# Kernel optimization log

Hardware: AMD Instinct MI355X
Metric: run time of the kernel (lower is better)

## Reference

```python
import jax, jax.numpy as jnp
import numpy as np

N_NODES = 10000
N_EDGES = 160000
DIM_IN = 32
DIM_OUT = 64
DIM_EDGE_HIDDEN = 128
BOND_FDIM = 13


def setup_inputs() -> dict:
    key = jax.random.key(0)
    ks = jax.random.split(key, 10)
    s = 0.1
    x = jax.random.normal(ks[0], (N_NODES, DIM_IN), dtype=jnp.float32)
    edge_index = jax.random.randint(ks[1], (2, N_EDGES), 0, N_NODES, dtype=jnp.int64)
    edge_attr = jax.random.uniform(ks[2], (N_EDGES, BOND_FDIM), dtype=jnp.float32)
    # edge-MLP params: BOND_FDIM -> hidden -> in*out
    W1 = jax.random.normal(ks[3], (BOND_FDIM, DIM_EDGE_HIDDEN), dtype=jnp.float32) * s
    b1 = jnp.zeros((DIM_EDGE_HIDDEN,), dtype=jnp.float32)
    W2 = jax.random.normal(ks[4], (DIM_EDGE_HIDDEN, DIM_IN * DIM_OUT), dtype=jnp.float32) * s
    b2 = jnp.zeros((DIM_IN * DIM_OUT,), dtype=jnp.float32)
    # NNConv root weight + bias
    root = jax.random.normal(ks[5], (DIM_IN, DIM_OUT), dtype=jnp.float32) * s
    bias = jnp.zeros((DIM_OUT,), dtype=jnp.float32)
    return {"x": x, "edge_index": edge_index, "edge_attr": edge_attr,
            "W1": W1, "b1": b1, "W2": W2, "b2": b2, "root": root, "bias": bias}


def reference(x, edge_index, edge_attr, W1, b1, W2, b2, root, bias):
    src, dst = edge_index[0], edge_index[1]  # PyG: row=source j, col=target i
    # edge MLP -> per-edge weight matrix [E, in, out]
    h = jax.nn.relu(edge_attr @ W1 + b1)
    w = (h @ W2 + b2).reshape(-1, DIM_IN, DIM_OUT)
    # gather source features, per-edge matmul -> messages [E, out]
    msg = jnp.einsum('ei,eio->eo', x[src], w)
    # scatter-add to target nodes
    agg = jax.ops.segment_sum(msg, dst, num_segments=N_NODES)
    out = agg + x @ root + bias
    return jax.nn.relu(out)
```

## Files before the change

kernel.cpp:

```cpp
#include <hip/hip_runtime.h>

#define N_NODES 10000
#define N_EDGES 160000
#define DIM_IN 32
#define DIM_OUT 64
#define DIM_HID 128
#define BOND 13
#define NB 16
#define NGROUPS (N_NODES / NB)
#define CAP 96

typedef _Float16 half2_t __attribute__((ext_vector_type(2)));
typedef _Float16 f16x8 __attribute__((ext_vector_type(8)));
typedef float f32x4 __attribute__((ext_vector_type(4)));
typedef unsigned int uint;

static __device__ __forceinline__ uint packh2(float a, float b) {
    half2_t h;
    h.x = (_Float16)a; h.y = (_Float16)b;
    return __builtin_bit_cast(uint, h);
}

static __device__ __forceinline__ int swz(int o, int kp) { return (o + kp) & 63; }

struct EScr {
    _Float16 ea16[16][32];
    _Float16 hbuf16[16][136];
};

__global__ void prep_kernel(const float* __restrict__ W2, uint4* __restrict__ W2p,
                            const float* __restrict__ W1, uint4* __restrict__ W1p,
                            const int* __restrict__ ei, int* __restrict__ cnt,
                            uint* __restrict__ es,
                            const float* __restrict__ x, const float* __restrict__ root,
                            const float* __restrict__ bias, float* __restrict__ out) {
    int idx = blockIdx.x * 256 + threadIdx.x;
    if (idx < 512 * 64) {
        int f = idx >> 6, lane = idx & 63;
        int k = f >> 2, of = f & 3;
        int q = lane >> 4, l15 = lane & 15;
        const float* base = W2 + k * 2048 + q * 512 + of * 16 + l15;
        uint u0 = packh2(base[0],   base[64]);
        uint u1 = packh2(base[128], base[192]);
        uint u2 = packh2(base[256], base[320]);
        uint u3 = packh2(base[384], base[448]);
        W2p[idx] = make_uint4(u0, u1, u2, u3);
    }
    if (idx < 512) {
        int nh = idx >> 6, lane = idx & 63;
        int quad = lane >> 4, l15 = lane & 15;
        int col = nh * 16 + l15;
        uint u[4];
#pragma unroll
        for (int jp = 0; jp < 4; ++jp) {
            int k0 = quad * 8 + 2 * jp, k1 = k0 + 1;
            float f0 = (k0 < BOND) ? W1[k0 * DIM_HID + col] : 0.f;
            float f1 = (k1 < BOND) ? W1[k1 * DIM_HID + col] : 0.f;
            u[jp] = packh2(f0, f1);
        }
        W1p[idx] = make_uint4(u[0], u[1], u[2], u[3]);
    }
    if (idx < N_NODES * DIM_OUT) {
        int n = idx >> 6, o = idx & 63;
        float r = bias[o];
        const float* xn = x + n * DIM_IN;
#pragma unroll 8
        for (int i = 0; i < DIM_IN; ++i) r += xn[i] * root[i * DIM_OUT + o];
        out[idx] = r;
    }
    if (idx < N_EDGES) {
        int src = ei[idx];
        int dst = ei[N_EDGES + idx];
        int slot = atomicAdd(&cnt[src], 1);
        if (slot < CAP)
            es[src * CAP + slot] = ((uint)dst << 18) | (uint)idx;
    }
}

__global__ __launch_bounds__(1024)
__attribute__((amdgpu_waves_per_eu(4, 4)))
void phase1_kernel(
    const float* __restrict__ x,
    const float* __restrict__ ea, const uint4* __restrict__ W1p,
    const float* __restrict__ b1, const uint4* __restrict__ W2p,
    const float* __restrict__ b2, const int* __restrict__ cnt,
    const uint* __restrict__ es, float* __restrict__ out)
{
    __shared__ uint  PhH[NB][DIM_HID / 4][DIM_OUT];
    __shared__ uint4 w1lds[8][64];

    const int t  = threadIdx.x;
    const int o  = t & 63;
    const int w  = t >> 6;
    const int n0 = blockIdx.x * NB;
    const int l15  = o & 15;
    const int quad = o >> 4;
    const int nd = w;
    const int n  = n0 + nd;

    if (t < 512) w1lds[t >> 6][t & 63] = W1p[t];

    const int start = n * CAP;
    int deg = cnt[n];
    uint pk = 0;
    if (o < 16) pk = es[start + o];

    f16x8 af;
    {
        uint ua[4];
        const float* xn8 = x + (long)(n0 + l15) * DIM_IN;
#pragma unroll
        for (int jj = 0; jj < 4; ++jj)
            ua[jj] = packh2(xn8[quad * 8 + 2 * jj], xn8[quad * 8 + 2 * jj + 1]);
        af = __builtin_bit_cast(f16x8, make_uint4(ua[0], ua[1], ua[2], ua[3]));
    }

    deg = deg < CAP ? deg : CAP;
    float eav[4];
    {
        const int tcnt0 = deg < 16 ? deg : 16;
#pragma unroll
        for (int r = 0; r < 4; ++r) {
            const int p = quad + 4 * r;
            const uint epk = __shfl(pk, p);
            eav[r] = 0.f;
            if (p < tcnt0 && l15 < BOND)
                eav[r] = ea[(long)(epk & 0x3FFFFu) * BOND + l15];
        }
    }

    f16x8 pregf[16];
    const int of = w & 3;
    const int ks = w >> 2;
#pragma unroll
    for (int h = 0; h < 2; ++h) {
        const int oo = of * 16 + l15;
        const int kbase = h * 64 + ks * 16;
#pragma unroll 2
        for (int m = 0; m < 8; ++m) {
            const int k0 = kbase + 2 * m;
            const uint4 bu0 = W2p[(k0 * 4 + of) * 64 + o];
            const uint4 bu1 = W2p[((k0 + 1) * 4 + of) * 64 + o];
            f32x4 D0 = {0.f, 0.f, 0.f, 0.f};
            f32x4 D1 = {0.f, 0.f, 0.f, 0.f};
            D0 = __builtin_amdgcn_mfma_f32_16x16x32_f16(
                     af, __builtin_bit_cast(f16x8, bu0), D0, 0, 0, 0);
            D1 = __builtin_amdgcn_mfma_f32_16x16x32_f16(
                     af, __builtin_bit_cast(f16x8, bu1), D1, 0, 0, 0);
            const int kpg = (kbase >> 1) + m;
            const int kpl = kpg & 31;
            const int sc = swz(oo, kpg);
#pragma unroll
            for (int r = 0; r < 4; ++r)
                PhH[quad * 4 + r][kpl][sc] = packh2(D0[r], D1[r]);
        }
        __syncthreads();
#pragma unroll
        for (int nt = 0; nt < 4; ++nt)
#pragma unroll
            for (int kh = 0; kh < 2; ++kh) {
                const int kk = 2 * h + kh;
                const int col = nt * 16 + l15;
                const int kpl = kh * 16 + quad * 4;
                const int kpg = h * 32 + kpl;
                uint4 u;
                u.x = PhH[nd][kpl + 0][swz(col, kpg + 0)];
                u.y = PhH[nd][kpl + 1][swz(col, kpg + 1)];
                u.z = PhH[nd][kpl + 2][swz(col, kpg + 2)];
                u.w = PhH[nd][kpl + 3][swz(col, kpg + 3)];
                pregf[nt * 4 + kk] = __builtin_bit_cast(f16x8, u);
            }
        __syncthreads();
    }

    float qv[4] = {0.f, 0.f, 0.f, 0.f};
    {
        const float* xn = x + (long)n * DIM_IN;
#pragma unroll 4
        for (int i = 0; i < DIM_IN; ++i) {
            float xv = xn[i];
#pragma unroll
            for (int nt = 0; nt < 4; ++nt)
                qv[nt] += xv * b2[i * DIM_OUT + nt * 16 + l15];
        }
    }

    float b1v[8];
#pragma unroll
    for (int nh = 0; nh < 8; ++nh) b1v[nh] = b1[nh * 16 + l15];

    EScr* S = (EScr*)((char*)&PhH[0][0][0] + nd * 8192);

    ((uint4*)S->ea16)[o] = make_uint4(0u, 0u, 0u, 0u);
    __builtin_amdgcn_wave_barrier();

    const int ntiles = (deg + 15) >> 4;
#pragma unroll 1
    for (int tb = 0; tb < ntiles; ++tb) {
        const int tilebase = tb * 16;
        const int tcnt = (deg - tilebase < 16) ? (deg - tilebase) : 16;
        __builtin_amdgcn_wave_barrier();
        if (l15 < BOND) {
#pragma unroll
            for (int r = 0; r < 4; ++r) {
                const int p = quad + 4 * r;
                if (p < tcnt) S->ea16[p][l15] = (_Float16)eav[r];
            }
        }
        __builtin_amdgcn_wave_barrier();
        const uint pkc = pk;

        uint pk2 = 0;
        float eav2[4] = {0.f, 0.f, 0.f, 0.f};
        const int tb2 = tilebase + 16;
        if (tb2 < deg) {
            const int tcnt2 = (deg - tb2 < 16) ? (deg - tb2) : 16;
            if (o < 16) pk2 = es[start + tb2 + o];
#pragma unroll
            for (int r = 0; r < 4; ++r) {
                const int p = quad + 4 * r;
                const uint epk = __shfl(pk2, p);
                if (p < tcnt2 && l15 < BOND)
                    eav2[r] = ea[(long)(epk & 0x3FFFFu) * BOND + l15];
            }
        }

        uint woff = 0;
        asm volatile("" : "+v"(woff));
        const int wo = (o + (int)woff) & 63;
        const f16x8 aef = *(const f16x8*)&S->ea16[l15][quad * 8];
#pragma unroll
        for (int nh = 0; nh < 8; ++nh) {
            const f16x8 wf = __builtin_bit_cast(f16x8, w1lds[nh][wo]);
            f32x4 hacc = {0.f, 0.f, 0.f, 0.f};
            hacc = __builtin_amdgcn_mfma_f32_16x16x32_f16(aef, wf, hacc, 0, 0, 0);
#pragma unroll
            for (int r = 0; r < 4; ++r) {
                float hv = hacc[r] + b1v[nh];
                S->hbuf16[quad * 4 + r][nh * 16 + l15] =
                    (_Float16)(hv > 0.f ? hv : 0.f);
            }
        }
        __builtin_amdgcn_wave_barrier();
        f16x8 hf[4];
#pragma unroll
        for (int kk = 0; kk < 4; ++kk)
            hf[kk] = *(const f16x8*)&S->hbuf16[l15][kk * 32 + quad * 8];
#pragma unroll
        for (int nt = 0; nt < 4; ++nt) {
            f32x4 acc = {0.f, 0.f, 0.f, 0.f};
#pragma unroll
            for (int kk = 0; kk < 4; ++kk)
                acc = __builtin_amdgcn_mfma_f32_16x16x32_f16(
                          hf[kk], pregf[nt * 4 + kk], acc, 0, 0, 0);
#pragma unroll
            for (int r = 0; r < 4; ++r) {
                const int p = quad * 4 + r;
                const uint dpk = __shfl(pkc, p);
                if (p < tcnt)
                    atomicAdd(&out[(long)(dpk >> 18) * DIM_OUT + nt * 16 + l15],
                              acc[r] + qv[nt]);
            }
        }
        pk = pk2;
#pragma unroll
        for (int r = 0; r < 4; ++r) eav[r] = eav2[r];
    }
}

__global__ __launch_bounds__(256) void relu_kernel(float* __restrict__ out) {
    int idx = blockIdx.x * 256 + threadIdx.x;
    if (idx < N_NODES * DIM_OUT) {
        float v = out[idx];
        out[idx] = v > 0.f ? v : 0.f;
    }
}


extern "C" void kernel_launch(void* const* d_in, const int* in_sizes, int n_in,
                              void* d_out, int out_size, void* d_ws, size_t ws_size,
                              hipStream_t stream) {
    const float* x    = (const float*)d_in[0];
    const int*   ei   = (const int*)d_in[1];
    const float* ea   = (const float*)d_in[2];
    const float* W1   = (const float*)d_in[3];
    const float* b1   = (const float*)d_in[4];
    const float* W2   = (const float*)d_in[5];
    const float* b2   = (const float*)d_in[6];
    const float* root = (const float*)d_in[7];
    const float* bias = (const float*)d_in[8];
    float* out = (float*)d_out;
    char* ws = (char*)d_ws;

    int*   cnt = (int*)(ws + 0);
    uint*  es  = (uint*)(ws + 40064);
    uint4* W2p = (uint4*)(ws + 3880064);
    uint4* W1p = (uint4*)(ws + 4404352);

    hipMemsetAsync(cnt, 0, 40064, stream);
    prep_kernel<<<2500, 256, 0, stream>>>(W2, W2p, W1, W1p, ei, cnt, es,
                                          x, root, bias, out);
    phase1_kernel<<<NGROUPS, 1024, 0, stream>>>(x, ea, W1p, b1, W2p, b2,
                                                cnt, es, out);
    relu_kernel<<<2500, 256, 0, stream>>>(out);
}
```

Baseline: 171.0 us.

## Fuse prep, edge conv and relu into one persistent kernel with grid barriers

Replaces the three kernel launches with a single persistent kernel of 256 blocks. Software grid barriers separate the prep phase (weight packing, edge bucketing) from a phase that pulls node groups from an atomic work counter, and then from a final phase that adds the root/bias term and applies relu. Messages now accumulate into a separate zeroed buffer instead of into the output, which needs a larger memset. This removes launch gaps and dynamically balances node groups, at the cost of spin-wait barriers, a larger memset, and relying on all 256 blocks being co-resident.

```diff
diff --git a/kernel.cpp b/kernel.cpp
--- a/kernel.cpp
+++ b/kernel.cpp
@@ -9,6 +9,7 @@
 #define NB 16
 #define NGROUPS (N_NODES / NB)
 #define CAP 96
+#define NBLK 256
 
 typedef _Float16 half2_t __attribute__((ext_vector_type(2)));
 typedef _Float16 f16x8 __attribute__((ext_vector_type(8)));
@@ -28,251 +29,265 @@
     _Float16 hbuf16[16][136];
 };
 
-__global__ void prep_kernel(const float* __restrict__ W2, uint4* __restrict__ W2p,
-                            const float* __restrict__ W1, uint4* __restrict__ W1p,
-                            const int* __restrict__ ei, int* __restrict__ cnt,
-                            uint* __restrict__ es,
-                            const float* __restrict__ x, const float* __restrict__ root,
-                            const float* __restrict__ bias, float* __restrict__ out) {
-    int idx = blockIdx.x * 256 + threadIdx.x;
-    if (idx < 512 * 64) {
-        int f = idx >> 6, lane = idx & 63;
-        int k = f >> 2, of = f & 3;
-        int q = lane >> 4, l15 = lane & 15;
-        const float* base = W2 + k * 2048 + q * 512 + of * 16 + l15;
-        uint u0 = packh2(base[0],   base[64]);
-        uint u1 = packh2(base[128], base[192]);
-        uint u2 = packh2(base[256], base[320]);
-        uint u3 = packh2(base[384], base[448]);
-        W2p[idx] = make_uint4(u0, u1, u2, u3);
+static __device__ __forceinline__ void gbar(int* ctr) {
+    __threadfence();
+    __syncthreads();
+    if (threadIdx.x == 0) {
+        atomicAdd(ctr, 1);
+        while (atomicAdd(ctr, 0) < NBLK) __builtin_amdgcn_s_sleep(16);
     }
-    if (idx < 512) {
-        int nh = idx >> 6, lane = idx & 63;
-        int quad = lane >> 4, l15 = lane & 15;
-        int col = nh * 16 + l15;
-        uint u[4];
-#pragma unroll
-        for (int jp = 0; jp < 4; ++jp) {
-            int k0 = quad * 8 + 2 * jp, k1 = k0 + 1;
-            float f0 = (k0 < BOND) ? W1[k0 * DIM_HID + col] : 0.f;
-            float f1 = (k1 < BOND) ? W1[k1 * DIM_HID + col] : 0.f;
-            u[jp] = packh2(f0, f1);
-        }
-        W1p[idx] = make_uint4(u[0], u[1], u[2], u[3]);
-    }
-    if (idx < N_NODES * DIM_OUT) {
-        int n = idx >> 6, o = idx & 63;
-        float r = bias[o];
-        const float* xn = x + n * DIM_IN;
-#pragma unroll 8
-        for (int i = 0; i < DIM_IN; ++i) r += xn[i] * root[i * DIM_OUT + o];
-        out[idx] = r;
-    }
-    if (idx < N_EDGES) {
-        int src = ei[idx];
-        int dst = ei[N_EDGES + idx];
-        int slot = atomicAdd(&cnt[src], 1);
-        if (slot < CAP)
-            es[src * CAP + slot] = ((uint)dst << 18) | (uint)idx;
-    }
+    __syncthreads();
+    __threadfence();
 }
 
 __global__ __launch_bounds__(1024)
 __attribute__((amdgpu_waves_per_eu(4, 4)))
-void phase1_kernel(
-    const float* __restrict__ x,
-    const float* __restrict__ ea, const uint4* __restrict__ W1p,
-    const float* __restrict__ b1, const uint4* __restrict__ W2p,
-    const float* __restrict__ b2, const int* __restrict__ cnt,
-    const uint* __restrict__ es, float* __restrict__ out)
+void fused_kernel(
+    const float* __restrict__ x,  const int* __restrict__ ei,
+    const float* __restrict__ ea, const float* __restrict__ W1,
+    const float* __restrict__ b1, const float* __restrict__ W2,
+    const float* __restrict__ b2, const float* __restrict__ root,
+    const float* __restrict__ bias,
+    int* __restrict__ ctrl, int* __restrict__ cnt,
+    float* __restrict__ accbuf, uint* __restrict__ es,
+    uint4* __restrict__ W2p, uint4* __restrict__ W1p,
+    float* __restrict__ out)
 {
     __shared__ uint  PhH[NB][DIM_HID / 4][DIM_OUT];
     __shared__ uint4 w1lds[8][64];
+    __shared__ int   gsh;
 
     const int t  = threadIdx.x;
     const int o  = t & 63;
     const int w  = t >> 6;
-    const int n0 = blockIdx.x * NB;
     const int l15  = o & 15;
     const int quad = o >> 4;
     const int nd = w;
-    const int n  = n0 + nd;
+
+    {
+        const int idx = blockIdx.x * 1024 + t;
+        if (idx < 512 * 64) {
+            int f = idx >> 6, lane = idx & 63;
+            int k = f >> 2, of = f & 3;
+            int q = lane >> 4, l = lane & 15;
+            const float* base = W2 + k * 2048 + q * 512 + of * 16 + l;
+            uint u0 = packh2(base[0],   base[64]);
+            uint u1 = packh2(base[128], base[192]);
+            uint u2 = packh2(base[256], base[320]);
+            uint u3 = packh2(base[384], base[448]);
+            W2p[idx] = make_uint4(u0, u1, u2, u3);
+        }
+        if (idx < 512) {
+            int nh = idx >> 6, lane = idx & 63;
+            int q = lane >> 4, l = lane & 15;
+            int col = nh * 16 + l;
+            uint u[4];
+#pragma unroll
+            for (int jp = 0; jp < 4; ++jp) {
+                int k0 = q * 8 + 2 * jp, k1 = k0 + 1;
+                float f0 = (k0 < BOND) ? W1[k0 * DIM_HID + col] : 0.f;
+                float f1 = (k1 < BOND) ? W1[k1 * DIM_HID + col] : 0.f;
+                u[jp] = packh2(f0, f1);
+            }
+            W1p[idx] = make_uint4(u[0], u[1], u[2], u[3]);
+        }
+        if (idx < N_EDGES) {
+            int src = ei[idx];
+            int dst = ei[N_EDGES + idx];
+            int slot = atomicAdd(&cnt[src], 1);
+            if (slot < CAP)
+                es[src * CAP + slot] = ((uint)dst << 18) | (uint)idx;
+        }
+    }
+    gbar(&ctrl[0]);
 
     if (t < 512) w1lds[t >> 6][t & 63] = W1p[t];
-
-    const int start = n * CAP;
-    int deg = cnt[n];
-    uint pk = 0;
-    if (o < 16) pk = es[start + o];
-
-    f16x8 af;
-    {
-        uint ua[4];
-        const float* xn8 = x + (long)(n0 + l15) * DIM_IN;
-#pragma unroll
-        for (int jj = 0; jj < 4; ++jj)
-            ua[jj] = packh2(xn8[quad * 8 + 2 * jj], xn8[quad * 8 + 2 * jj + 1]);
-        af = __builtin_bit_cast(f16x8, make_uint4(ua[0], ua[1], ua[2], ua[3]));
-    }
-
-    deg = deg < CAP ? deg : CAP;
-    float eav[4];
-    {
-        const int tcnt0 = deg < 16 ? deg : 16;
-#pragma unroll
-        for (int r = 0; r < 4; ++r) {
-            const int p = quad + 4 * r;
-            const uint epk = __shfl(pk, p);
-            eav[r] = 0.f;
-            if (p < tcnt0 && l15 < BOND)
-                eav[r] = ea[(long)(epk & 0x3FFFFu) * BOND + l15];
-        }
-    }
-
-    f16x8 pregf[16];
+    float b1v[8];
+#pragma unroll
+    for (int nh = 0; nh < 8; ++nh) b1v[nh] = b1[nh * 16 + l15];
     const int of = w & 3;
     const int ks = w >> 2;
-#pragma unroll
-    for (int h = 0; h < 2; ++h) {
-        const int oo = of * 16 + l15;
-        const int kbase = h * 64 + ks * 16;
-#pragma unroll 2
-        for (int m = 0; m < 8; ++m) {
-            const int k0 = kbase + 2 * m;
-            const uint4 bu0 = W2p[(k0 * 4 + of) * 64 + o];
-            const uint4 bu1 = W2p[((k0 + 1) * 4 + of) * 64 + o];
-            f32x4 D0 = {0.f, 0.f, 0.f, 0.f};
-            f32x4 D1 = {0.f, 0.f, 0.f, 0.f};
-            D0 = __builtin_amdgcn_mfma_f32_16x16x32_f16(
-                     af, __builtin_bit_cast(f16x8, bu0), D0, 0, 0, 0);
-            D1 = __builtin_amdgcn_mfma_f32_16x16x32_f16(
-                     af, __builtin_bit_cast(f16x8, bu1), D1, 0, 0, 0);
-            const int kpg = (kbase >> 1) + m;
-            const int kpl = kpg & 31;
-            const int sc = swz(oo, kpg);
-#pragma unroll
-            for (int r = 0; r < 4; ++r)
-                PhH[quad * 4 + r][kpl][sc] = packh2(D0[r], D1[r]);
-        }
+
+    for (;;) {
         __syncthreads();
-#pragma unroll
-        for (int nt = 0; nt < 4; ++nt)
-#pragma unroll
-            for (int kh = 0; kh < 2; ++kh) {
-                const int kk = 2 * h + kh;
-                const int col = nt * 16 + l15;
-                const int kpl = kh * 16 + quad * 4;
-                const int kpg = h * 32 + kpl;
-                uint4 u;
-                u.x = PhH[nd][kpl + 0][swz(col, kpg + 0)];
-                u.y = PhH[nd][kpl + 1][swz(col, kpg + 1)];
-                u.z = PhH[nd][kpl + 2][swz(col, kpg + 2)];
-                u.w = PhH[nd][kpl + 3][swz(col, kpg + 3)];
-                pregf[nt * 4 + kk] = __builtin_bit_cast(f16x8, u);
-            }
+        if (t == 0) gsh = atomicAdd(&ctrl[2], 1);
         __syncthreads();
-    }
-
-    float qv[4] = {0.f, 0.f, 0.f, 0.f};
-    {
-        const float* xn = x + (long)n * DIM_IN;
-#pragma unroll 4
-        for (int i = 0; i < DIM_IN; ++i) {
-            float xv = xn[i];
-#pragma unroll
-            for (int nt = 0; nt < 4; ++nt)
-                qv[nt] += xv * b2[i * DIM_OUT + nt * 16 + l15];
-        }
-    }
-
-    float b1v[8];
-#pragma unroll
-    for (int nh = 0; nh < 8; ++nh) b1v[nh] = b1[nh * 16 + l15];
-
-    EScr* S = (EScr*)((char*)&PhH[0][0][0] + nd * 8192);
-
-    ((uint4*)S->ea16)[o] = make_uint4(0u, 0u, 0u, 0u);
-    __builtin_amdgcn_wave_barrier();
-
-    const int ntiles = (deg + 15) >> 4;
-#pragma unroll 1
-    for (int tb = 0; tb < ntiles; ++tb) {
-        const int tilebase = tb * 16;
-        const int tcnt = (deg - tilebase < 16) ? (deg - tilebase) : 16;
-        __builtin_amdgcn_wave_barrier();
-        if (l15 < BOND) {
+        const int g = gsh;
+        if (g >= NGROUPS) break;
+        const int n0 = g * NB;
+        const int n  = n0 + nd;
+
+        const int start = n * CAP;
+        int deg = cnt[n];
+        uint pk = 0;
+        if (o < 16) pk = es[start + o];
+
+        f16x8 af;
+        {
+            uint ua[4];
+            const float* xn8 = x + (long)(n0 + l15) * DIM_IN;
+#pragma unroll
+            for (int jj = 0; jj < 4; ++jj)
+                ua[jj] = packh2(xn8[quad * 8 + 2 * jj], xn8[quad * 8 + 2 * jj + 1]);
+            af = __builtin_bit_cast(f16x8, make_uint4(ua[0], ua[1], ua[2], ua[3]));
+        }
+
+        deg = deg < CAP ? deg : CAP;
+        float eav[4];
+        {
+            const int tcnt0 = deg < 16 ? deg : 16;
 #pragma unroll
             for (int r = 0; r < 4; ++r) {
                 const int p = quad + 4 * r;
-                if (p < tcnt) S->ea16[p][l15] = (_Float16)eav[r];
-            }
-        }
+                const uint epk = __shfl(pk, p);
+                eav[r] = 0.f;
+                if (p < tcnt0 && l15 < BOND)
+                    eav[r] = ea[(long)(epk & 0x3FFFFu) * BOND + l15];
+            }
+        }
+
+        f16x8 pregf[16];
+#pragma unroll
+        for (int h = 0; h < 2; ++h) {
+            const int oo = of * 16 + l15;
+            const int kbase = h * 64 + ks * 16;
+#pragma unroll 2
+            for (int m = 0; m < 8; ++m) {
+                const int k0 = kbase + 2 * m;
+                const uint4 bu0 = W2p[(k0 * 4 + of) * 64 + o];
+                const uint4 bu1 = W2p[((k0 + 1) * 4 + of) * 64 + o];
+                f32x4 D0 = {0.f, 0.f, 0.f, 0.f};
+                f32x4 D1 = {0.f, 0.f, 0.f, 0.f};
+                D0 = __builtin_amdgcn_mfma_f32_16x16x32_f16(
+                         af, __builtin_bit_cast(f16x8, bu0), D0, 0, 0, 0);
+                D1 = __builtin_amdgcn_mfma_f32_16x16x32_f16(
+                         af, __builtin_bit_cast(f16x8, bu1), D1, 0, 0, 0);
+                const int kpg = (kbase >> 1) + m;
+                const int kpl = kpg & 31;
+                const int sc = swz(oo, kpg);
+#pragma unroll
+                for (int r = 0; r < 4; ++r)
+                    PhH[quad * 4 + r][kpl][sc] = packh2(D0[r], D1[r]);
+            }
+            __syncthreads();
+#pragma unroll
+            for (int nt = 0; nt < 4; ++nt)
+#pragma unroll
+                for (int kh = 0; kh < 2; ++kh) {
+                    const int kk = 2 * h + kh;
+                    const int col = nt * 16 + l15;
+                    const int kpl = kh * 16 + quad * 4;
+                    const int kpg = h * 32 + kpl;
+                    uint4 u;
+                    u.x = PhH[nd][kpl + 0][swz(col, kpg + 0)];
+                    u.y = PhH[nd][kpl + 1][swz(col, kpg + 1)];
+                    u.z = PhH[nd][kpl + 2][swz(col, kpg + 2)];
+                    u.w = PhH[nd][kpl + 3][swz(col, kpg + 3)];
+                    pregf[nt * 4 + kk] = __builtin_bit_cast(f16x8, u);
+                }
+            __syncthreads();
+        }
+
+        float qv[4] = {0.f, 0.f, 0.f, 0.f};
+        {
+            const float* xn = x + (long)n * DIM_IN;
+#pragma unroll 4
+            for (int i = 0; i < DIM_IN; ++i) {
+                float xv = xn[i];
+#pragma unroll
+                for (int nt = 0; nt < 4; ++nt)
+                    qv[nt] += xv * b2[i * DIM_OUT + nt * 16 + l15];
+            }
+        }
+
+        EScr* S = (EScr*)((char*)&PhH[0][0][0] + nd * 8192);
+
+        ((uint4*)S->ea16)[o] = make_uint4(0u, 0u, 0u, 0u);
         __builtin_amdgcn_wave_barrier();
-        const uint pkc = pk;
-
-        uint pk2 = 0;
-        float eav2[4] = {0.f, 0.f, 0.f, 0.f};
-        const int tb2 = tilebase + 16;
-        if (tb2 < deg) {
-            const int tcnt2 = (deg - tb2 < 16) ? (deg - tb2) : 16;
-            if (o < 16) pk2 = es[start + tb2 + o];
-#pragma unroll
-            for (int r = 0; r < 4; ++r) {
-                const int p = quad + 4 * r;
-                const uint epk = __shfl(pk2, p);
-                if (p < tcnt2 && l15 < BOND)
-                    eav2[r] = ea[(long)(epk & 0x3FFFFu) * BOND + l15];
-            }
-        }
-
-        uint woff = 0;
-        asm volatile("" : "+v"(woff));
-        const int wo = (o + (int)woff) & 63;
-        const f16x8 aef = *(const f16x8*)&S->ea16[l15][quad * 8];
-#pragma unroll
-        for (int nh = 0; nh < 8; ++nh) {
-            const f16x8 wf = __builtin_bit_cast(f16x8, w1lds[nh][wo]);
-            f32x4 hacc = {0.f, 0.f, 0.f, 0.f};
-            hacc = __builtin_amdgcn_mfma_f32_16x16x32_f16(aef, wf, hacc, 0, 0, 0);
-#pragma unroll
-            for (int r = 0; r < 4; ++r) {
-                float hv = hacc[r] + b1v[nh];
-                S->hbuf16[quad * 4 + r][nh * 16 + l15] =
-                    (_Float16)(hv > 0.f ? hv : 0.f);
-            }
-        }
-        __builtin_amdgcn_wave_barrier();
-        f16x8 hf[4];
-#pragma unroll
-        for (int kk = 0; kk < 4; ++kk)
-            hf[kk] = *(const f16x8*)&S->hbuf16[l15][kk * 32 + quad * 8];
-#pragma unroll
-        for (int nt = 0; nt < 4; ++nt) {
-            f32x4 acc = {0.f, 0.f, 0.f, 0.f};
+
+        const int ntiles = (deg + 15) >> 4;
+#pragma unroll 1
+        for (int tb = 0; tb < ntiles; ++tb) {
+            const int tilebase = tb * 16;
+            const int tcnt = (deg - tilebase < 16) ? (deg - tilebase) : 16;
+            __builtin_amdgcn_wave_barrier();
+            if (l15 < BOND) {
+#pragma unroll
+                for (int r = 0; r < 4; ++r) {
+                    const int p = quad + 4 * r;
+                    if (p < tcnt) S->ea16[p][l15] = (_Float16)eav[r];
+                }
+            }
+            __builtin_amdgcn_wave_barrier();
+            const uint pkc = pk;
+
+            uint pk2 = 0;
+            float eav2[4] = {0.f, 0.f, 0.f, 0.f};
+            const int tb2 = tilebase + 16;
+            if (tb2 < deg) {
+                const int tcnt2 = (deg - tb2 < 16) ? (deg - tb2) : 16;
+                if (o < 16) pk2 = es[start + tb2 + o];
+#pragma unroll
+                for (int r = 0; r < 4; ++r) {
+                    const int p = quad + 4 * r;
+                    const uint epk = __shfl(pk2, p);
+                    if (p < tcnt2 && l15 < BOND)
+                        eav2[r] = ea[(long)(epk & 0x3FFFFu) * BOND + l15];
+                }
+            }
+
+            uint woff = 0;
+            asm volatile("" : "+v"(woff));
+            const int wo = (o + (int)woff) & 63;
+            const f16x8 aef = *(const f16x8*)&S->ea16[l15][quad * 8];
+#pragma unroll
+            for (int nh = 0; nh < 8; ++nh) {
+                const f16x8 wf = __builtin_bit_cast(f16x8, w1lds[nh][wo]);
+                f32x4 hacc = {0.f, 0.f, 0.f, 0.f};
+                hacc = __builtin_amdgcn_mfma_f32_16x16x32_f16(aef, wf, hacc, 0, 0, 0);
+#pragma unroll
+                for (int r = 0; r < 4; ++r) {
+                    float hv = hacc[r] + b1v[nh];
+                    S->hbuf16[quad * 4 + r][nh * 16 + l15] =
+                        (_Float16)(hv > 0.f ? hv : 0.f);
+                }
+            }
+            __builtin_amdgcn_wave_barrier();
+            f16x8 hf[4];
 #pragma unroll
             for (int kk = 0; kk < 4; ++kk)
-                acc = __builtin_amdgcn_mfma_f32_16x16x32_f16(
-                          hf[kk], pregf[nt * 4 + kk], acc, 0, 0, 0);
-#pragma unroll
-            for (int r = 0; r < 4; ++r) {
-                const int p = quad * 4 + r;
-                const uint dpk = __shfl(pkc, p);
-                if (p < tcnt)
-                    atomicAdd(&out[(long)(dpk >> 18) * DIM_OUT + nt * 16 + l15],
-                              acc[r] + qv[nt]);
-            }
-        }
-        pk = pk2;
-#pragma unroll
-        for (int r = 0; r < 4; ++r) eav[r] = eav2[r];
+                hf[kk] = *(const f16x8*)&S->hbuf16[l15][kk * 32 + quad * 8];
+#pragma unroll
+            for (int nt = 0; nt < 4; ++nt) {
+                f32x4 acc = {0.f, 0.f, 0.f, 0.f};
+#pragma unroll
+                for (int kk = 0; kk < 4; ++kk)
+                    acc = __builtin_amdgcn_mfma_f32_16x16x32_f16(
+                              hf[kk], pregf[nt * 4 + kk], acc, 0, 0, 0);
+#pragma unroll
+                for (int r = 0; r < 4; ++r) {
+                    const int p = quad * 4 + r;
+                    const uint dpk = __shfl(pkc, p);
+                    if (p < tcnt)
+                        atomicAdd(&accbuf[(long)(dpk >> 18) * DIM_OUT + nt * 16 + l15],
+                                  acc[r] + qv[nt]);
+                }
+            }
+            pk = pk2;
+#pragma unroll
+            for (int r = 0; r < 4; ++r) eav[r] = eav2[r];
+        }
     }
-}
-
-__global__ __launch_bounds__(256) void relu_kernel(float* __restrict__ out) {
-    int idx = blockIdx.x * 256 + threadIdx.x;
-    if (idx < N_NODES * DIM_OUT) {
-        float v = out[idx];
-        out[idx] = v > 0.f ? v : 0.f;
+    gbar(&ctrl[1]);
+
+    for (int idx = blockIdx.x * 1024 + t; idx < N_NODES * DIM_OUT;
+         idx += NBLK * 1024) {
+        const int nn = idx >> 6, oo = idx & 63;
+        float r = bias[oo] + accbuf[idx];
+        const float* xn = x + (long)nn * DIM_IN;
+#pragma unroll 8
+        for (int i = 0; i < DIM_IN; ++i) r += xn[i] * root[i * DIM_OUT + oo];
+        out[idx] = r > 0.f ? r : 0.f;
     }
 }
 
@@ -292,15 +307,14 @@
     float* out = (float*)d_out;
     char* ws = (char*)d_ws;
 
-    int*   cnt = (int*)(ws + 0);
-    uint*  es  = (uint*)(ws + 40064);
-    uint4* W2p = (uint4*)(ws + 3880064);
-    uint4* W1p = (uint4*)(ws + 4404352);
-
-    hipMemsetAsync(cnt, 0, 40064, stream);
-    prep_kernel<<<2500, 256, 0, stream>>>(W2, W2p, W1, W1p, ei, cnt, es,
-                                          x, root, bias, out);
-    phase1_kernel<<<NGROUPS, 1024, 0, stream>>>(x, ea, W1p, b1, W2p, b2,
-                                                cnt, es, out);
-    relu_kernel<<<2500, 256, 0, stream>>>(out);
+    int*   ctrl   = (int*)(ws + 0);
+    int*   cnt    = (int*)(ws + 64);
+    float* accbuf = (float*)(ws + 40128);
+    uint*  es     = (uint*)(ws + 2600128);
+    uint4* W2p    = (uint4*)(ws + 6440128);
+    uint4* W1p    = (uint4*)(ws + 6964416);
+
+    hipMemsetAsync(ws, 0, 2600128, stream);
+    fused_kernel<<<NBLK, 1024, 0, stream>>>(x, ei, ea, W1, b1, W2, b2, root, bias,
+                                            ctrl, cnt, accbuf, es, W2p, W1p, out);
 }
```

Result: slower. 559.8 us (+227.3%).
